# Kernel optimization log

Hardware: AMD Instinct MI355X
Metric: run time of the kernel (lower is better)

## Reference

```python
import jax, jax.numpy as jnp
import numpy as np

N_NODES = 100000
N_EDGES = 1600000
IN = 128
OUT = 32
HEADS = 4
NEG_SLOPE = 0.2


def setup_inputs() -> dict:
    key = jax.random.key(0)
    ks = jax.random.split(key, 6)
    x = jax.random.normal(ks[0], (N_NODES, IN), dtype=jnp.float32)
    row = jax.random.randint(ks[1], (N_EDGES,), 0, N_NODES, dtype=jnp.int32)
    col = jax.random.randint(ks[2], (N_EDGES,), 0, N_NODES, dtype=jnp.int32)
    W = jax.random.normal(ks[3], (OUT * HEADS, IN), dtype=jnp.float32) * (1.0 / np.sqrt(IN))
    b = jnp.zeros((OUT * HEADS,), dtype=jnp.float32)
    a_l = jax.random.normal(ks[4], (1, OUT, HEADS), dtype=jnp.float32) * 0.1
    a_r = jax.random.normal(ks[5], (1, OUT, HEADS), dtype=jnp.float32) * 0.1
    return {"x": x, "row": row, "col": col, "W": W, "b": b, "a_l": a_l, "a_r": a_r}


def reference(x, row, col, W, b, a_l, a_r):
    N = x.shape[0]
    # Z: [N, OUT, HEADS] (row-major view of [N, OUT*HEADS], matching torch .view)
    Z = (x @ W.T + b).reshape(N, OUT, HEADS)
    e_l = jnp.sum(Z * a_l, axis=1)  # [N, HEADS]
    e_r = jnp.sum(Z * a_r, axis=1)  # [N, HEADS]
    e = e_l[row] + e_r[col]         # [E, HEADS]
    e = jnp.where(e > 0, e, NEG_SLOPE * e)  # LeakyReLU
    # segment softmax over edges grouped by destination (row)
    m = jax.ops.segment_max(e, row, num_segments=N)      # [N, HEADS]
    ex = jnp.exp(e - m[row])                              # [E, HEADS]
    denom = jax.ops.segment_sum(ex, row, num_segments=N)  # [N, HEADS]
    alpha = ex / denom[row]                               # [E, HEADS]
    # bspmm: out[i,:,h] = sum_{(i,j) in E} alpha[e,h] * Z[j,:,h]
    out = jax.ops.segment_sum(alpha[:, None, :] * Z[col], row, num_segments=N)
    return out
```

## Files before the change

kernel.cpp:

```cpp
#include <hip/hip_runtime.h>
#include <hip/hip_bf16.h>
#include <math.h>


typedef __attribute__((ext_vector_type(8))) short bf16x8;
typedef __attribute__((ext_vector_type(4))) float f32x4;

__device__ __forceinline__ ushort f2bf(float f) {
  __hip_bfloat16 h = __float2bfloat16(f);
  return __builtin_bit_cast(ushort, h);
}
__device__ __forceinline__ float bf2f(ushort u) {
  unsigned v = ((unsigned)u) << 16;
  return __builtin_bit_cast(float, v);
}

__global__ __launch_bounds__(512) void prep0(
    const float* __restrict__ W, ushort* __restrict__ Wh,
    ushort* __restrict__ Wl, int* __restrict__ deg, int N) {
  int i = blockIdx.x * 512 + threadIdx.x;
  if (i < 16384) {
    float w = W[i];
    ushort hb = f2bf(w);
    Wh[i] = hb;
    Wl[i] = f2bf(w - bf2f(hb));
  }
  if (i < N) deg[i] = 0;
}

__global__ __launch_bounds__(512, 4) void gemm_deg(
    const float* __restrict__ x, const ushort* __restrict__ Wh,
    const ushort* __restrict__ Wl, const float* __restrict__ bias,
    const float* __restrict__ a_l, const float* __restrict__ a_r,
    ushort* __restrict__ Zh, float* __restrict__ el, float* __restrict__ er,
    int N, const int* __restrict__ row, int* __restrict__ deg,
    int* __restrict__ rank, int E, int G1) {
  __shared__ __align__(16) ushort smem[16896];
  __shared__ float sal[128], sar[128];

  if ((int)blockIdx.x >= G1) {
    int e = ((int)blockIdx.x - G1) * 512 + threadIdx.x;
    if (e < E) rank[e] = atomicAdd(&deg[row[e]], 1);
    return;
  }

  const int t = threadIdx.x;
  const int lane = t & 63;
  const int wv = t >> 6;
  const int row0 = blockIdx.x * 128;
  const int l15 = lane & 15, l4 = lane >> 4;
  const int ch = wv * 16 + l15;

  if (t < 128) { sal[t] = a_l[t]; sar[t] = a_r[t]; }

  bf16x8 Bh[4], Bl[4];
#pragma unroll
  for (int kf = 0; kf < 4; ++kf) {
    int off = ch * 128 + kf * 32 + l4 * 8;
    Bh[kf] = *(const bf16x8*)&Wh[off];
    Bl[kf] = *(const bf16x8*)&Wl[off];
  }

  ushort* xh = smem;
#pragma unroll
  for (int i = 0; i < 8; ++i) {
    int f4 = i * 512 + t;
    int r = f4 >> 5;
    int k = (f4 & 31) * 4;
    int gr = row0 + r;
    float4 v = make_float4(0.f, 0.f, 0.f, 0.f);
    if (gr < N) v = ((const float4*)x)[(size_t)gr * 32 + (f4 & 31)];
    int idx = r * 128 + (k ^ ((r & 7) << 3));
    uint2 hv;
    hv.x = f2bf(v.x) | ((unsigned)f2bf(v.y) << 16);
    hv.y = f2bf(v.z) | ((unsigned)f2bf(v.w) << 16);
    *(uint2*)&xh[idx] = hv;
  }
  __syncthreads();

  f32x4 acc[8];
#pragma unroll
  for (int rt = 0; rt < 8; ++rt) acc[rt] = (f32x4){0.f, 0.f, 0.f, 0.f};

#pragma unroll
  for (int kf = 0; kf < 4; ++kf) {
#pragma unroll
    for (int rt = 0; rt < 8; ++rt) {
      int r = rt * 16 + l15;
      int idx = r * 128 + ((kf * 32 + l4 * 8) ^ ((r & 7) << 3));
      bf16x8 ah = *(const bf16x8*)&xh[idx];
      acc[rt] = __builtin_amdgcn_mfma_f32_16x16x32_bf16(ah, Bh[kf], acc[rt], 0, 0, 0);
      acc[rt] = __builtin_amdgcn_mfma_f32_16x16x32_bf16(ah, Bl[kf], acc[rt], 0, 0, 0);
    }
  }
  __syncthreads();

  ushort* zs = smem;
  {
    float bv = bias[ch];
    int o = ch >> 2, h = ch & 3;
    int s = (o & 15) * 8 + h * 2 + (o >> 4);
#pragma unroll
    for (int rt = 0; rt < 8; ++rt) {
#pragma unroll
      for (int j = 0; j < 4; ++j) {
        int r = rt * 16 + l4 * 4 + j;
        zs[r * 132 + s] = f2bf(acc[rt][j] + bv);
      }
    }
  }
  __syncthreads();

  {
    int r = t >> 2;
    int h = t & 3;
    int gr = row0 + r;
    if (gr < N) {
#pragma unroll
      for (int q = 0; q < 4; ++q) {
        uint4 v = *(const uint4*)&zs[r * 132 + h * 32 + q * 8];
        *(uint4*)&Zh[(size_t)gr * 128 + h * 32 + q * 8] = v;
      }
      float sl = 0.f, sr = 0.f;
#pragma unroll
      for (int op = 0; op < 16; ++op) {
        unsigned zz = *(const unsigned*)&zs[r * 132 + op * 8 + h * 2];
        float zlo = bf2f((ushort)(zz & 0xffff));
        float zhi = bf2f((ushort)(zz >> 16));
        int c = (op << 2) + h;
        sl += zlo * sal[c] + zhi * sal[c + 64];
        sr += zlo * sar[c] + zhi * sar[c + 64];
      }
      el[(unsigned)gr * 4 + h] = sl;
      er[(unsigned)gr * 4 + h] = sr;
    }
  }
}

__global__ __launch_bounds__(256) void scan1(
    const int* __restrict__ deg, int* __restrict__ base,
    int* __restrict__ bsum, int N) {
  __shared__ int s[256];
  int i = blockIdx.x * 256 + threadIdx.x;
  int v = (i < N) ? deg[i] : 0;
  s[threadIdx.x] = v;
  __syncthreads();
#pragma unroll
  for (int off = 1; off < 256; off <<= 1) {
    int t = (threadIdx.x >= off) ? s[threadIdx.x - off] : 0;
    __syncthreads();
    s[threadIdx.x] += t;
    __syncthreads();
  }
  if (i < N) base[i] = s[threadIdx.x] - v;
  if (threadIdx.x == 255) bsum[blockIdx.x] = s[255];
}

__global__ __launch_bounds__(512) void scan2(int* __restrict__ bsum, int NB) {
  __shared__ int s[512];
  int v = (threadIdx.x < NB) ? bsum[threadIdx.x] : 0;
  s[threadIdx.x] = v;
  __syncthreads();
#pragma unroll
  for (int off = 1; off < 512; off <<= 1) {
    int t = (threadIdx.x >= off) ? s[threadIdx.x - off] : 0;
    __syncthreads();
    s[threadIdx.x] += t;
    __syncthreads();
  }
  if (threadIdx.x < NB) bsum[threadIdx.x] = s[threadIdx.x] - v;
}

__global__ __launch_bounds__(256) void fill(
    const int* __restrict__ row, const int* __restrict__ col,
    const int* __restrict__ rank, const int* __restrict__ base,
    const int* __restrict__ bsum, int* __restrict__ sorted_col, int E) {
  int e = blockIdx.x * 256 + threadIdx.x;
  if (e < E) {
    int r = row[e];
    sorted_col[base[r] + bsum[r >> 8] + rank[e]] = col[e];
  }
}

__global__ __launch_bounds__(256) void gather(
    const int* __restrict__ base, const int* __restrict__ bsum,
    const int* __restrict__ deg, const int* __restrict__ sorted_col,
    const float* __restrict__ el, const float* __restrict__ er,
    const ushort* __restrict__ Zh, float* __restrict__ out, int N) {
  int t = threadIdx.x;
  int lane = t & 63;
  int n = blockIdx.x * 4 + (t >> 6);
  if (n >= N) return;
  int h = lane & 3;
  int jj = lane >> 2;
  int s = base[n] + bsum[n >> 8];
  int d = deg[n];
  int end = s + d;
  float elv = el[((unsigned)n << 2) + h];
  float acc0 = 0.f, acc1 = 0.f, sumA = 0.f;
  const unsigned* Zh32 = (const unsigned*)Zh;
  const unsigned zlane = (unsigned)lane;
  const int bpb = (lane & 3) << 2;

  for (int p = s; p < end; p += 16) {
    int cnt = end - p;
    int cl6 = 0;
    float xv = 0.f;
    if (jj < cnt) {
      int cl = sorted_col[p + jj];
      float e = elv + er[((unsigned)cl << 2) + h];
      e = fmaxf(e, 0.2f * e);
      xv = __expf(e);
      cl6 = cl << 6;
    }
    sumA += xv;
    float xvb[16];
    unsigned addr[16];
#pragma unroll
    for (int q = 0; q < 16; ++q) {
      int a = bpb + (q << 4);
      xvb[q] = __builtin_bit_cast(float,
          __builtin_amdgcn_ds_bpermute(a, __builtin_bit_cast(int, xv)));
      addr[q] = (unsigned)__builtin_amdgcn_ds_bpermute(a, cl6) + zlane;
    }
    unsigned zz[16];
#pragma unroll
    for (int q = 0; q < 16; ++q) zz[q] = Zh32[addr[q]];
#pragma unroll
    for (int q = 0; q < 16; ++q) {
      acc0 = fmaf(xvb[q], __builtin_bit_cast(float, zz[q] << 16), acc0);
      acc1 = fmaf(xvb[q], __builtin_bit_cast(float, zz[q] & 0xffff0000u), acc1);
    }
  }
  float sum = sumA;
  sum += __shfl_xor(sum, 4, 64);
  sum += __shfl_xor(sum, 8, 64);
  sum += __shfl_xor(sum, 16, 64);
  sum += __shfl_xor(sum, 32, 64);
  float inv = (d > 0) ? 1.0f / sum : 0.f;
  unsigned ob = ((unsigned)n << 7) + zlane;
  __builtin_nontemporal_store(acc0 * inv, &out[ob]);
  __builtin_nontemporal_store(acc1 * inv, &out[ob + 64]);
}

extern "C" void kernel_launch(void* const* d_in, const int* in_sizes, int n_in,
                              void* d_out, int out_size, void* d_ws, size_t ws_size,
                              hipStream_t stream) {
  const float* x   = (const float*)d_in[0];
  const int*   row = (const int*)d_in[1];
  const int*   col = (const int*)d_in[2];
  const float* W   = (const float*)d_in[3];
  const float* b   = (const float*)d_in[4];
  const float* a_l = (const float*)d_in[5];
  const float* a_r = (const float*)d_in[6];
  float* out = (float*)d_out;

  const int N = in_sizes[0] / 128;
  const int E = in_sizes[1];
  const int NB = (N + 255) / 256;

  char* w = (char*)d_ws;
  ushort* Zh       = (ushort*)w;             w += (size_t)N * 128 * 2;
  int*   sorted_col= (int*)w;                w += (size_t)E * 4;
  int*   rank      = (int*)w;                w += (size_t)E * 4;
  float* el        = (float*)w;              w += (size_t)N * 4 * 4;
  float* er        = (float*)w;              w += (size_t)N * 4 * 4;
  int*   deg       = (int*)w;                w += (size_t)N * 4;
  int*   base      = (int*)w;                w += (size_t)N * 4;
  int*   bsum      = (int*)w;                w += 512 * 4;
  ushort* Wh       = (ushort*)w;             w += 16384 * 2;
  ushort* Wl       = (ushort*)w;             w += 16384 * 2;

  const int P0 = (N > 16384 ? N : 16384);
  prep0<<<(P0 + 511) / 512, 512, 0, stream>>>(W, Wh, Wl, deg, N);

  const int G1 = (N + 127) / 128;
  const int G2 = (E + 511) / 512;
  gemm_deg<<<G1 + G2, 512, 0, stream>>>(x, Wh, Wl, b, a_l, a_r, Zh, el, er,
                                        N, row, deg, rank, E, G1);

  scan1<<<NB, 256, 0, stream>>>(deg, base, bsum, N);
  scan2<<<1, 512, 0, stream>>>(bsum, NB);
  fill<<<(E + 255) / 256, 256, 0, stream>>>(row, col, rank, base, bsum,
                                            sorted_col, E);
  gather<<<(N + 3) / 4, 256, 0, stream>>>(base, bsum, deg, sorted_col, el, er,
                                          Zh, out, N);
}
```

Before: 195.2 us.

## Privatize degree counters into eight copies and split histogram from GEMM kernel

Degree counting now uses eight privatized counter arrays, chosen by block index, to reduce atomic contention on per-node counters. The edge-histogram work moves out of the GEMM launch into its own kernel, and a new scan kernel merges the eight copies into per-copy offsets plus the node degree. Fill adds the per-copy offset when placing each edge. In exchange there is an extra launch, the GEMM and histogram no longer overlap, and the counter buffer is eight times larger, which means more memory traffic for zeroing and scanning.

```diff
diff --git a/kernel.cpp b/kernel.cpp
--- a/kernel.cpp
+++ b/kernel.cpp
@@ -17,7 +17,7 @@
 
 __global__ __launch_bounds__(512) void prep0(
     const float* __restrict__ W, ushort* __restrict__ Wh,
-    ushort* __restrict__ Wl, int* __restrict__ deg, int N) {
+    ushort* __restrict__ Wl, int* __restrict__ cntP, int N8) {
   int i = blockIdx.x * 512 + threadIdx.x;
   if (i < 16384) {
     float w = W[i];
@@ -25,24 +25,17 @@
     Wh[i] = hb;
     Wl[i] = f2bf(w - bf2f(hb));
   }
-  if (i < N) deg[i] = 0;
-}
-
-__global__ __launch_bounds__(512, 4) void gemm_deg(
+  if (i < N8) cntP[i] = 0;
+}
+
+__global__ __launch_bounds__(512, 4) void gemm_z(
     const float* __restrict__ x, const ushort* __restrict__ Wh,
     const ushort* __restrict__ Wl, const float* __restrict__ bias,
     const float* __restrict__ a_l, const float* __restrict__ a_r,
     ushort* __restrict__ Zh, float* __restrict__ el, float* __restrict__ er,
-    int N, const int* __restrict__ row, int* __restrict__ deg,
-    int* __restrict__ rank, int E, int G1) {
+    int N) {
   __shared__ __align__(16) ushort smem[16896];
   __shared__ float sal[128], sar[128];
-
-  if ((int)blockIdx.x >= G1) {
-    int e = ((int)blockIdx.x - G1) * 512 + threadIdx.x;
-    if (e < E) rank[e] = atomicAdd(&deg[row[e]], 1);
-    return;
-  }
 
   const int t = threadIdx.x;
   const int lane = t & 63;
@@ -137,23 +130,46 @@
   }
 }
 
-__global__ __launch_bounds__(256) void scan1(
-    const int* __restrict__ deg, int* __restrict__ base,
+__global__ __launch_bounds__(256) void deg_rank(
+    const int* __restrict__ row, int* __restrict__ cntP,
+    int* __restrict__ rank, int E, int N) {
+  int e = blockIdx.x * 256 + threadIdx.x;
+  if (e >= E) return;
+  int copy = blockIdx.x & 7;
+  rank[e] = atomicAdd(&cntP[copy * N + row[e]], 1);
+}
+
+__global__ __launch_bounds__(256) void nscan(
+    int* __restrict__ cntP, int* __restrict__ deg, int* __restrict__ base,
     int* __restrict__ bsum, int N) {
-  __shared__ int s[256];
-  int i = blockIdx.x * 256 + threadIdx.x;
-  int v = (i < N) ? deg[i] : 0;
-  s[threadIdx.x] = v;
+  __shared__ int ss[256];
+  int t = threadIdx.x;
+  int i = blockIdx.x * 256 + t;
+  int tot = 0;
+  if (i < N) {
+    int run = 0;
+#pragma unroll
+    for (int k = 0; k < 8; ++k) {
+      int c = cntP[k * N + i];
+      cntP[k * N + i] = run;
+      run += c;
+    }
+    tot = run;
+  }
+  ss[t] = tot;
   __syncthreads();
 #pragma unroll
   for (int off = 1; off < 256; off <<= 1) {
-    int t = (threadIdx.x >= off) ? s[threadIdx.x - off] : 0;
+    int u = (t >= off) ? ss[t - off] : 0;
     __syncthreads();
-    s[threadIdx.x] += t;
+    ss[t] += u;
     __syncthreads();
   }
-  if (i < N) base[i] = s[threadIdx.x] - v;
-  if (threadIdx.x == 255) bsum[blockIdx.x] = s[255];
+  if (i < N) {
+    base[i] = ss[t] - tot;
+    deg[i] = tot;
+  }
+  if (t == 255) bsum[blockIdx.x] = ss[255];
 }
 
 __global__ __launch_bounds__(512) void scan2(int* __restrict__ bsum, int NB) {
@@ -174,12 +190,14 @@
 __global__ __launch_bounds__(256) void fill(
     const int* __restrict__ row, const int* __restrict__ col,
     const int* __restrict__ rank, const int* __restrict__ base,
-    const int* __restrict__ bsum, int* __restrict__ sorted_col, int E) {
+    const int* __restrict__ bsum, const int* __restrict__ cntP,
+    int* __restrict__ sorted_col, int E, int N) {
   int e = blockIdx.x * 256 + threadIdx.x;
-  if (e < E) {
-    int r = row[e];
-    sorted_col[base[r] + bsum[r >> 8] + rank[e]] = col[e];
-  }
+  if (e >= E) return;
+  int r = row[e];
+  int copy = (e >> 8) & 7;
+  int pos = base[r] + bsum[r >> 8] + cntP[copy * N + r] + rank[e];
+  sorted_col[pos] = col[e];
 }
 
 __global__ __launch_bounds__(256) void gather(
@@ -203,10 +221,10 @@
   const int bpb = (lane & 3) << 2;
 
   for (int p = s; p < end; p += 16) {
-    int cnt = end - p;
+    int vn = end - p;
     int cl6 = 0;
     float xv = 0.f;
-    if (jj < cnt) {
+    if (jj < vn) {
       int cl = sorted_col[p + jj];
       float e = elv + er[((unsigned)cl << 2) + h];
       e = fmaxf(e, 0.2f * e);
@@ -265,24 +283,24 @@
   int*   rank      = (int*)w;                w += (size_t)E * 4;
   float* el        = (float*)w;              w += (size_t)N * 4 * 4;
   float* er        = (float*)w;              w += (size_t)N * 4 * 4;
+  int*   cntP      = (int*)w;                w += (size_t)N * 8 * 4;
   int*   deg       = (int*)w;                w += (size_t)N * 4;
   int*   base      = (int*)w;                w += (size_t)N * 4;
   int*   bsum      = (int*)w;                w += 512 * 4;
   ushort* Wh       = (ushort*)w;             w += 16384 * 2;
   ushort* Wl       = (ushort*)w;             w += 16384 * 2;
 
-  const int P0 = (N > 16384 ? N : 16384);
-  prep0<<<(P0 + 511) / 512, 512, 0, stream>>>(W, Wh, Wl, deg, N);
-
-  const int G1 = (N + 127) / 128;
-  const int G2 = (E + 511) / 512;
-  gemm_deg<<<G1 + G2, 512, 0, stream>>>(x, Wh, Wl, b, a_l, a_r, Zh, el, er,
-                                        N, row, deg, rank, E, G1);
-
-  scan1<<<NB, 256, 0, stream>>>(deg, base, bsum, N);
+  const int N8 = N * 8;
+  const int P0 = (N8 > 16384 ? N8 : 16384);
+  prep0<<<(P0 + 511) / 512, 512, 0, stream>>>(W, Wh, Wl, cntP, N8);
+
+  gemm_z<<<(N + 127) / 128, 512, 0, stream>>>(x, Wh, Wl, b, a_l, a_r,
+                                              Zh, el, er, N);
+  deg_rank<<<(E + 255) / 256, 256, 0, stream>>>(row, cntP, rank, E, N);
+  nscan<<<NB, 256, 0, stream>>>(cntP, deg, base, bsum, N);
   scan2<<<1, 512, 0, stream>>>(bsum, NB);
-  fill<<<(E + 255) / 256, 256, 0, stream>>>(row, col, rank, base, bsum,
-                                            sorted_col, E);
+  fill<<<(E + 255) / 256, 256, 0, stream>>>(row, col, rank, base, bsum, cntP,
+                                            sorted_col, E, N);
   gather<<<(N + 3) / 4, 256, 0, stream>>>(base, bsum, deg, sorted_col, el, er,
                                           Zh, out, N);
 }
```

New measurement: 209.7 us. 7.4% more time.
